# Optimization experiments

Measured on AMD Instinct MI355X. Metric: run time of the kernel, lower is better.

The kernel has to match this reference:

```python
import jax, jax.numpy as jnp
import numpy as np

H, HID = 2, 64
N_USER, N_POST, N_ENT = 50000, 100000, 20000
EDGES = [("publish", 100000, N_USER, N_POST), ("repost", 200000, N_USER, N_POST), ("contain", 200000, N_POST, N_ENT), ("interact", 400000, N_USER, N_USER), ("follow", 400000, N_USER, N_USER), ("similar", 250000, N_POST, N_POST)]


def setup_inputs() -> dict:
    key = jax.random.key(0)
    ks = iter(jax.random.split(key, 64))
    d = {}
    d["x_post"] = jax.random.normal(next(ks), (N_POST, 768), jnp.float32)
    d["x_user"] = jax.random.normal(next(ks), (N_USER, 32), jnp.float32)
    d["x_entity"] = jax.random.normal(next(ks), (N_ENT, 64), jnp.float32)
    for name, E, ns, nd in EDGES:
        d["src_" + name] = jax.random.randint(next(ks), (E,), 0, ns, jnp.int32)
        d["dst_" + name] = jax.random.randint(next(ks), (E,), 0, nd, jnp.int32)
    def lin(k, o, i):
        return jax.random.normal(k, (o, i), jnp.float32) / np.sqrt(i)
    d["post_proj_w"] = lin(next(ks), HID, 768); d["post_proj_b"] = jnp.zeros((HID,), jnp.float32)
    d["user_proj_w"] = lin(next(ks), HID, 32); d["user_proj_b"] = jnp.zeros((HID,), jnp.float32)
    d["ent_proj_w"] = lin(next(ks), HID, 64); d["ent_proj_b"] = jnp.zeros((HID,), jnp.float32)
    # 2 layers x 6 relations of bipartite GATConv params, stacked
    d["W_src"] = jax.random.normal(next(ks), (2, 6, H * HID, HID), jnp.float32) / np.sqrt(HID)
    d["W_dst"] = jax.random.normal(next(ks), (2, 6, H * HID, HID), jnp.float32) / np.sqrt(HID)
    d["a_src"] = jax.random.normal(next(ks), (2, 6, H, HID), jnp.float32) * 0.1
    d["a_dst"] = jax.random.normal(next(ks), (2, 6, H, HID), jnp.float32) * 0.1
    d["gat_b"] = jnp.zeros((2, 6, HID), jnp.float32)
    d["cls_w1"] = lin(next(ks), HID // 2, HID); d["cls_b1"] = jnp.zeros((HID // 2,), jnp.float32)
    d["cls_w2"] = lin(next(ks), 1, HID // 2); d["cls_b2"] = jnp.zeros((1,), jnp.float32)
    return d


def _gat(x_src, x_dst, src, dst, w_s, w_d, a_s, a_d, b):
    """PyG GATConv, bipartite, heads=H, concat=False, no self loops."""
    n_dst = x_dst.shape[0]
    hs = (x_src @ w_s.T).reshape(-1, H, HID)   # [N_src, H, C]
    hd = (x_dst @ w_d.T).reshape(-1, H, HID)   # [N_dst, H, C]
    al_s = jnp.einsum("nhc,hc->nh", hs, a_s)
    al_d = jnp.einsum("nhc,hc->nh", hd, a_d)
    e = jax.nn.leaky_relu(al_s[src] + al_d[dst], negative_slope=0.2)  # [E, H]
    m = jax.ops.segment_max(e, dst, num_segments=n_dst)
    m = jnp.where(jnp.isfinite(m), m, 0.0)  # empty segments -> -inf, unused
    p = jnp.exp(e - m[dst])
    s = jax.ops.segment_sum(p, dst, num_segments=n_dst)
    alpha = p / (s[dst] + 1e-16)
    out = jax.ops.segment_sum(hs[src] * alpha[:, :, None], dst, num_segments=n_dst)
    return out.mean(axis=1) + b  # concat=False -> mean over heads, plus bias


def reference(x_post, x_user, x_entity, src_publish, dst_publish, src_repost, dst_repost, src_contain, dst_contain, src_interact, dst_interact, src_follow, dst_follow, src_similar, dst_similar, post_proj_w, post_proj_b, user_proj_w, user_proj_b, ent_proj_w, ent_proj_b, W_src, W_dst, a_src, a_dst, gat_b, cls_w1, cls_b1, cls_w2, cls_b2):
    h_post = x_post @ post_proj_w.T + post_proj_b
    h_user = x_user @ user_proj_w.T + user_proj_b
    h_ent = x_entity @ ent_proj_w.T + ent_proj_b
    for l in range(2):
        def g(r, xs, xd, s, dd):
            return _gat(xs, xd, s, dd, W_src[l, r], W_dst[l, r], a_src[l, r], a_dst[l, r], gat_b[l, r])
        new_post = (g(0, h_user, h_post, src_publish, dst_publish)
                    + g(1, h_user, h_post, src_repost, dst_repost)
                    + g(5, h_post, h_post, src_similar, dst_similar))
        new_ent = g(2, h_post, h_ent, src_contain, dst_contain)
        new_user = (g(3, h_user, h_user, src_interact, dst_interact)
                    + g(4, h_user, h_user, src_follow, dst_follow))
        h_post, h_user, h_ent = jax.nn.relu(new_post), jax.nn.relu(new_user), jax.nn.relu(new_ent)
    h = jax.nn.relu(h_post @ cls_w1.T + cls_b1)  # dropout is eval-mode identity
    return (h @ cls_w2.T + cls_b2).squeeze(-1)
```

## Files before the change

kernel.cpp:

```cpp
#include <hip/hip_runtime.h>

#define NPOST 100000
#define NUSER 50000
#define NENT  20000
#define NDTOT 420000
#define ETOT  1550000
#define NSCANBLK 206
#define NT_AL 150000

typedef short short8 __attribute__((ext_vector_type(8)));
typedef float f32x4 __attribute__((ext_vector_type(4)));
typedef unsigned short ushort4v __attribute__((ext_vector_type(4)));

static __device__ __forceinline__ unsigned short f2bf(float x){
  union { float f; unsigned u; } v; v.f = x;
  unsigned r = v.u + 0x7FFF + ((v.u >> 16) & 1);
  return (unsigned short)(r >> 16);
}
static __device__ __forceinline__ float bf2f(unsigned short h){
  union { unsigned u; float f; } v; v.u = ((unsigned)h) << 16;
  return v.f;
}

struct EdgeMeta {
  const int* src[6];
  const int* dst[6];
  int E[6];
  int degoff[6];
};

struct PrepArgs {
  const float *Wp, *Wu, *We, *Wsrc, *Wdst, *asrc, *adst, *gatb;
  unsigned short *WpH, *WpL, *WuH, *WuL, *WeH, *WeL, *lbH, *lbL;
  float *weff_s, *weff_d, *bsum;
};

__global__ void k_prep(PrepArgs P){
  int idx = blockIdx.x * blockDim.x + threadIdx.x;
  if (idx < 49152){
    float x = P.Wp[idx];
    unsigned short h = f2bf(x);
    P.WpH[idx] = h; P.WpL[idx] = f2bf(x - bf2f(h));
  } else if (idx < 51200){
    int i = idx - 49152;
    float x = P.Wu[i];
    unsigned short h = f2bf(x);
    P.WuH[i] = h; P.WuL[i] = f2bf(x - bf2f(h));
  } else if (idx < 55296){
    int i = idx - 51200;
    float x = P.We[i];
    unsigned short h = f2bf(x);
    P.WeH[i] = h; P.WeL[i] = f2bf(x - bf2f(h));
  } else if (idx < 153600){
    int i = idx - 55296;
    const int off[6]  = {0, 24576, 40960, 49152, 73728, 90112};
    const int Ks[6]   = {384, 256, 128, 384, 256, 128};
    int seg = 5;
    #pragma unroll
    for (int s = 4; s >= 0; s--) if (i < off[s + 1]) seg = s;
    int l = seg / 3, type = seg % 3;
    int K = Ks[seg];
    int rem = i - off[seg];
    int n = rem / K, k = rem - n * K;
    int slot = k >> 7, head = (k >> 6) & 1, kk = k & 63;
    int rel;
    if (type == 0)      rel = (slot == 0) ? 0 : (slot == 1 ? 1 : 5);
    else if (type == 1) rel = (slot == 0) ? 3 : 4;
    else                rel = 2;
    int m = l * 6 + rel;
    float x = P.Wsrc[(size_t)m * 8192 + (head * 64 + n) * 64 + kk];
    unsigned short h = f2bf(x);
    P.lbH[i] = h; P.lbL[i] = f2bf(x - bf2f(h));
  } else if (idx < 156672){
    int i = idx - 153600;
    const float* W; const float* a; float* o; int j;
    if (i < 1536){ W = P.Wsrc; a = P.asrc; o = P.weff_s; j = i; }
    else         { W = P.Wdst; a = P.adst; o = P.weff_d; j = i - 1536; }
    int m = j >> 7;
    int rem = j & 127;
    int hh = rem >> 6, k = rem & 63;
    const float* Wm = W + (size_t)m * 8192;
    const float* am = a + (size_t)m * 128;
    float acc = 0.f;
    #pragma unroll 8
    for (int c = 0; c < 64; c++)
      acc += Wm[(hh * 64 + c) * 64 + k] * am[hh * 64 + c];
    o[j] = acc;
  } else if (idx < 157056){
    int i = idx - 156672;
    int c = i & 63;
    int lt = i >> 6;
    int l = lt / 3, t = lt % 3;
    float v;
    if (t == 0)      v = P.gatb[(l*6+0)*64+c] + P.gatb[(l*6+1)*64+c] + P.gatb[(l*6+5)*64+c];
    else if (t == 1) v = P.gatb[(l*6+3)*64+c] + P.gatb[(l*6+4)*64+c];
    else             v = P.gatb[(l*6+2)*64+c];
    P.bsum[lt * 64 + c] = v;
  }
}


__global__ void k_hist(EdgeMeta em, int* __restrict__ deg){
  int r = blockIdx.y;
  int e = blockIdx.x * blockDim.x + threadIdx.x;
  if (e >= em.E[r]) return;
  atomicAdd(&deg[em.degoff[r] + em.dst[r][e]], 1);
}

__global__ __launch_bounds__(256) void k_scanA(const int* __restrict__ deg,
                                               int* __restrict__ rowstart,
                                               int* __restrict__ blocksum){
  __shared__ int sums[256];
  int t = threadIdx.x;
  int base = blockIdx.x * 2048 + t * 8;
  int v[8]; int s = 0;
  #pragma unroll
  for (int i = 0; i < 8; i++){
    int j = base + i;
    v[i] = (j < NDTOT) ? deg[j] : 0;
    s += v[i];
  }
  sums[t] = s;
  __syncthreads();
  for (int off = 1; off < 256; off <<= 1){
    int x = (t >= off) ? sums[t - off] : 0;
    __syncthreads();
    sums[t] += x;
    __syncthreads();
  }
  int excl = (t > 0) ? sums[t - 1] : 0;
  if (t == 255) blocksum[blockIdx.x] = sums[255];
  int run = excl;
  #pragma unroll
  for (int i = 0; i < 8; i++){
    int j = base + i;
    if (j < NDTOT) rowstart[j] = run;
    run += v[i];
  }
}

__global__ __launch_bounds__(256) void k_scanB(int* __restrict__ blocksum){
  __shared__ int s[256];
  int t = threadIdx.x;
  s[t] = (t < NSCANBLK) ? blocksum[t] : 0;
  __syncthreads();
  for (int off = 1; off < 256; off <<= 1){
    int x = (t >= off) ? s[t - off] : 0;
    __syncthreads();
    s[t] += x;
    __syncthreads();
  }
  int excl = (t > 0) ? s[t - 1] : 0;
  if (t < NSCANBLK) blocksum[t] = excl;
}

__global__ void k_scanC(int* __restrict__ rowstart, const int* __restrict__ blocksum,
                        int* __restrict__ cursor){
  int j = blockIdx.x * blockDim.x + threadIdx.x;
  if (j < NDTOT){
    int v = rowstart[j] + blocksum[j >> 11];
    rowstart[j] = v;
    cursor[j] = v;
  }
  if (j == 0) rowstart[NDTOT] = ETOT;
}

__global__ void k_scatter(EdgeMeta em, int* __restrict__ cursor,
                          int* __restrict__ csr_src, int* __restrict__ csr_row){
  int r = blockIdx.y;
  int e = blockIdx.x * blockDim.x + threadIdx.x;
  if (e >= em.E[r]) return;
  int d = em.dst[r][e];
  int w = em.degoff[r] + d;
  int pos = atomicAdd(&cursor[w], 1);
  csr_src[pos] = em.src[r][e];
  csr_row[pos] = w;
}


struct AlArgs {
  const float *h0, *h1;
  const float *ws, *wd;
  float *als, *ald;
  int layer;
};

static __device__ __forceinline__ float2 dot2w(const float4* hr, const float* __restrict__ w){
  const float4* w0 = (const float4*)w;
  const float4* w1 = (const float4*)(w + 64);
  float a0 = 0.f, a1 = 0.f;
  #pragma unroll
  for (int q = 0; q < 16; q++){
    float4 v = hr[q];
    float4 x0 = w0[q], x1 = w1[q];
    a0 += v.x*x0.x + v.y*x0.y + v.z*x0.z + v.w*x0.w;
    a1 += v.x*x1.x + v.y*x1.y + v.z*x1.z + v.w*x1.w;
  }
  return make_float2(a0, a1);
}

__global__ __launch_bounds__(256) void k_al_all(AlArgs A){
  int i = blockIdx.x * blockDim.x + threadIdx.x;
  if (i >= NT_AL) return;
  float4 hr[16];
  if (i < NPOST){
    int n = i;
    const float4* hp = (const float4*)(A.h0 + (size_t)n * 64);
    #pragma unroll
    for (int q = 0; q < 16; q++) hr[q] = hp[q];
    *(float2*)(A.als + (size_t)(300000 + n) * 2) = dot2w(hr, A.ws + 5 * 128);
    *(float2*)(A.ald + (size_t)(0      + n) * 2) = dot2w(hr, A.wd + 0 * 128);
    *(float2*)(A.ald + (size_t)(100000 + n) * 2) = dot2w(hr, A.wd + 1 * 128);
    *(float2*)(A.ald + (size_t)(320000 + n) * 2) = dot2w(hr, A.wd + 5 * 128);
  } else {
    int n = i - NPOST;
    const float4* hp = (const float4*)(A.h1 + (size_t)n * 64);
    #pragma unroll
    for (int q = 0; q < 16; q++) hr[q] = hp[q];
    *(float2*)(A.als + (size_t)(0      + n) * 2) = dot2w(hr, A.ws + 0 * 128);
    *(float2*)(A.als + (size_t)(50000  + n) * 2) = dot2w(hr, A.ws + 1 * 128);
    if (A.layer == 0){
      *(float2*)(A.als + (size_t)(200000 + n) * 2) = dot2w(hr, A.ws + 3 * 128);
      *(float2*)(A.als + (size_t)(250000 + n) * 2) = dot2w(hr, A.ws + 4 * 128);
      *(float2*)(A.ald + (size_t)(220000 + n) * 2) = dot2w(hr, A.wd + 3 * 128);
      *(float2*)(A.ald + (size_t)(270000 + n) * 2) = dot2w(hr, A.wd + 4 * 128);
    }
  }
}


struct EdgepArgs {
  const int *csr_src, *csr_row;
  const float *als, *ald;
  float2 *pcsr;
  int thr, off, nE;
};

__global__ __launch_bounds__(256) void k_edgep(EdgepArgs A){
  int e0 = blockIdx.x * blockDim.x + threadIdx.x;
  if (e0 >= A.nE) return;
  int e = e0 < A.thr ? e0 : e0 + A.off;
  int w = A.csr_row[e];
  int soffr;
  if      (w < 100000) soffr = 0;
  else if (w < 200000) soffr = 50000;
  else if (w < 220000) soffr = 100000;
  else if (w < 270000) soffr = 200000;
  else if (w < 320000) soffr = 250000;
  else                 soffr = 300000;
  int sidx = A.csr_src[e];
  float2 as = *(const float2*)(A.als + (size_t)(soffr + sidx) * 2);
  float2 ad = *(const float2*)(A.ald + (size_t)w * 2);
  float e0v = as.x + ad.x, e1v = as.y + ad.y;
  e0v = e0v > 0.f ? e0v : 0.2f * e0v;
  e1v = e1v > 0.f ? e1v : 0.2f * e1v;
  A.pcsr[e] = make_float2(__expf(e0v), __expf(e1v));
}


struct AggArgs {
  const int *rowstart, *csr_src;
  const float *h0, *h1;
  const float2 *pcsr;
  unsigned short *aH0, *aH1, *aL0, *aL1;
  int nrows, thr, off;
};

__global__ __launch_bounds__(256) void k_agg4(AggArgs A){
  int wv = (blockIdx.x * blockDim.x + threadIdx.x) >> 6;
  int lane = threadIdx.x & 63;
  int g = lane >> 4;
  int l16 = lane & 15;
  int r = wv * 4 + g;
  if (r >= A.nrows) return;
  int w = r < A.thr ? r : r + A.off;
  int dgor, slotr, stt, dtt;
  if      (w < 100000){ dgor = 0;      stt = 1; dtt = 0; slotr = 0; }
  else if (w < 200000){ dgor = 100000; stt = 1; dtt = 0; slotr = 1; }
  else if (w < 270000){ dgor = 220000; stt = 1; dtt = 1; slotr = 0; }
  else if (w < 320000){ dgor = 270000; stt = 1; dtt = 1; slotr = 1; }
  else                { dgor = 320000; stt = 0; dtt = 0; slotr = 2; }
  int row = w - dgor;
  const float* h = (stt == 0) ? A.h0 : A.h1;
  int rs = A.rowstart[w], re = A.rowstart[w + 1];
  f32x4 a0 = (f32x4){0.f,0.f,0.f,0.f};
  f32x4 a1 = (f32x4){0.f,0.f,0.f,0.f};
  float s0 = 0.f, s1 = 0.f;
  int e = rs;
  for (; e + 3 < re; e += 4){
    int sa = A.csr_src[e];
    int sb = A.csr_src[e + 1];
    int sc = A.csr_src[e + 2];
    int sd = A.csr_src[e + 3];
    float2 pa = A.pcsr[e];
    float2 pb = A.pcsr[e + 1];
    float2 pc = A.pcsr[e + 2];
    float2 pd = A.pcsr[e + 3];
    f32x4 ha = *(const f32x4*)(h + (size_t)sa * 64 + l16 * 4);
    f32x4 hb = *(const f32x4*)(h + (size_t)sb * 64 + l16 * 4);
    f32x4 hc = *(const f32x4*)(h + (size_t)sc * 64 + l16 * 4);
    f32x4 hd = *(const f32x4*)(h + (size_t)sd * 64 + l16 * 4);
    #pragma unroll
    for (int j = 0; j < 4; j++){
      a0[j] = fmaf(pa.x, ha[j], a0[j]);
      a1[j] = fmaf(pa.y, ha[j], a1[j]);
    }
    s0 += pa.x; s1 += pa.y;
    #pragma unroll
    for (int j = 0; j < 4; j++){
      a0[j] = fmaf(pb.x, hb[j], a0[j]);
      a1[j] = fmaf(pb.y, hb[j], a1[j]);
    }
    s0 += pb.x; s1 += pb.y;
    #pragma unroll
    for (int j = 0; j < 4; j++){
      a0[j] = fmaf(pc.x, hc[j], a0[j]);
      a1[j] = fmaf(pc.y, hc[j], a1[j]);
    }
    s0 += pc.x; s1 += pc.y;
    #pragma unroll
    for (int j = 0; j < 4; j++){
      a0[j] = fmaf(pd.x, hd[j], a0[j]);
      a1[j] = fmaf(pd.y, hd[j], a1[j]);
    }
    s0 += pd.x; s1 += pd.y;
  }
  for (; e + 1 < re; e += 2){
    int sa = A.csr_src[e];
    int sb = A.csr_src[e + 1];
    float2 pa = A.pcsr[e];
    float2 pb = A.pcsr[e + 1];
    f32x4 ha = *(const f32x4*)(h + (size_t)sa * 64 + l16 * 4);
    f32x4 hb = *(const f32x4*)(h + (size_t)sb * 64 + l16 * 4);
    #pragma unroll
    for (int j = 0; j < 4; j++){
      a0[j] = fmaf(pa.x, ha[j], a0[j]);
      a1[j] = fmaf(pa.y, ha[j], a1[j]);
    }
    s0 += pa.x; s1 += pa.y;
    #pragma unroll
    for (int j = 0; j < 4; j++){
      a0[j] = fmaf(pb.x, hb[j], a0[j]);
      a1[j] = fmaf(pb.y, hb[j], a1[j]);
    }
    s0 += pb.x; s1 += pb.y;
  }
  if (e < re){
    int sa = A.csr_src[e];
    float2 pa = A.pcsr[e];
    f32x4 ha = *(const f32x4*)(h + (size_t)sa * 64 + l16 * 4);
    #pragma unroll
    for (int j = 0; j < 4; j++){
      a0[j] = fmaf(pa.x, ha[j], a0[j]);
      a1[j] = fmaf(pa.y, ha[j], a1[j]);
    }
    s0 += pa.x; s1 += pa.y;
  }
  float r0 = s0 > 0.f ? 0.5f / s0 : 0.f;
  float r1 = s1 > 0.f ? 0.5f / s1 : 0.f;
  int K = (dtt == 0) ? 384 : 256;
  unsigned short* aH = (dtt == 0) ? A.aH0 : A.aH1;
  unsigned short* aL = (dtt == 0) ? A.aL0 : A.aL1;
  size_t base = (size_t)row * K + slotr * 128 + l16 * 4;
  ushort4v H0, H1, L0, L1;
  #pragma unroll
  for (int j = 0; j < 4; j++){
    float v0 = a0[j] * r0;
    float v1 = a1[j] * r1;
    unsigned short h0 = f2bf(v0); H0[j] = h0; L0[j] = f2bf(v0 - bf2f(h0));
    unsigned short h1 = f2bf(v1); H1[j] = h1; L1[j] = f2bf(v1 - bf2f(h1));
  }
  *(ushort4v*)(aH + base)      = H0;
  *(ushort4v*)(aH + base + 64) = H1;
  *(ushort4v*)(aL + base)      = L0;
  *(ushort4v*)(aL + base + 64) = L1;
}


static __device__ __forceinline__ int swz(int row, int k){
  return row * 32 + ((((k >> 3) ^ ((row >> 2) & 3))) << 3) + (k & 7);
}

struct GemmJob {
  const float* A32;
  const unsigned short* AH; const unsigned short* AL;
  const unsigned short* BH; const unsigned short* BL;
  const float* bias; float* C;
  int N; int K;
};
struct GemmJobs { GemmJob j0, j1, j2; int nb0, nb1; };

template<int ASRC, int RELU>
__global__ __launch_bounds__(256) void k_mfgemm3(GemmJobs G){
  __shared__ __align__(16) unsigned short sAh[128 * 32];
  __shared__ __align__(16) unsigned short sAl[128 * 32];
  __shared__ __align__(16) unsigned short sBh[64 * 32];
  __shared__ __align__(16) unsigned short sBl[64 * 32];
  int b = blockIdx.x;
  GemmJob jb = G.j0;
  int boff = 0;
  if (b >= G.nb1){ jb = G.j2; boff = G.nb1; }
  else if (b >= G.nb0){ jb = G.j1; boff = G.nb0; }
  const float* A32 = jb.A32;
  const unsigned short* AH = jb.AH;
  const unsigned short* AL = jb.AL;
  const unsigned short* BH = jb.BH;
  const unsigned short* BL = jb.BL;
  int N = jb.N, K = jb.K;

  int t = threadIdx.x;
  int w = t >> 6, lane = t & 63;
  int q = lane >> 4, m15 = lane & 15;
  int r0 = (b - boff) * 128;
  f32x4 acc[2][4];
  #pragma unroll
  for (int i = 0; i < 2; i++)
    #pragma unroll
    for (int j = 0; j < 4; j++)
      acc[i][j] = (f32x4){0.f, 0.f, 0.f, 0.f};

  int arow = t >> 1, akb = (t & 1) * 16;
  int brow = t >> 2, bkb = (t & 3) * 8;

  for (int k0 = 0; k0 < K; k0 += 32){
    int gr = r0 + arow;
    if (ASRC == 0){
      float v[16];
      if (gr < N){
        const float4* ap = (const float4*)(A32 + (size_t)gr * K + k0 + akb);
        #pragma unroll
        for (int i = 0; i < 4; i++){
          float4 f = ap[i];
          v[i*4+0] = f.x; v[i*4+1] = f.y; v[i*4+2] = f.z; v[i*4+3] = f.w;
        }
      } else {
        #pragma unroll
        for (int i = 0; i < 16; i++) v[i] = 0.f;
      }
      short8 h0, h1, l0, l1;
      #pragma unroll
      for (int i = 0; i < 8; i++){
        unsigned short hh = f2bf(v[i]);
        h0[i] = (short)hh; l0[i] = (short)f2bf(v[i] - bf2f(hh));
        unsigned short hj = f2bf(v[8+i]);
        h1[i] = (short)hj; l1[i] = (short)f2bf(v[8+i] - bf2f(hj));
      }
      *(short8*)(sAh + swz(arow, akb))     = h0;
      *(short8*)(sAh + swz(arow, akb + 8)) = h1;
      *(short8*)(sAl + swz(arow, akb))     = l0;
      *(short8*)(sAl + swz(arow, akb + 8)) = l1;
    } else {
      short8 h0 = {0,0,0,0,0,0,0,0}, h1 = {0,0,0,0,0,0,0,0};
      short8 l0 = {0,0,0,0,0,0,0,0}, l1 = {0,0,0,0,0,0,0,0};
      if (gr < N){
        const short8* hp = (const short8*)(AH + (size_t)gr * K + k0 + akb);
        const short8* lp = (const short8*)(AL + (size_t)gr * K + k0 + akb);
        h0 = hp[0]; h1 = hp[1];
        l0 = lp[0]; l1 = lp[1];
      }
      *(short8*)(sAh + swz(arow, akb))     = h0;
      *(short8*)(sAh + swz(arow, akb + 8)) = h1;
      *(short8*)(sAl + swz(arow, akb))     = l0;
      *(short8*)(sAl + swz(arow, akb + 8)) = l1;
    }
    {
      short8 bh = *(const short8*)(BH + (size_t)brow * K + k0 + bkb);
      short8 bl = *(const short8*)(BL + (size_t)brow * K + k0 + bkb);
      *(short8*)(sBh + swz(brow, bkb)) = bh;
      *(short8*)(sBl + swz(brow, bkb)) = bl;
    }
    __syncthreads();
    short8 ah[2], al_[2];
    #pragma unroll
    for (int i = 0; i < 2; i++){
      int mrow = w * 32 + i * 16 + m15;
      ah[i]  = *(const short8*)(sAh + swz(mrow, q * 8));
      al_[i] = *(const short8*)(sAl + swz(mrow, q * 8));
    }
    #pragma unroll
    for (int j = 0; j < 4; j++){
      int bn = j * 16 + m15;
      short8 bh = *(const short8*)(sBh + swz(bn, q * 8));
      short8 bl = *(const short8*)(sBl + swz(bn, q * 8));
      #pragma unroll
      for (int i = 0; i < 2; i++){
        acc[i][j] = __builtin_amdgcn_mfma_f32_16x16x32_bf16(ah[i],  bh, acc[i][j], 0, 0, 0);
        acc[i][j] = __builtin_amdgcn_mfma_f32_16x16x32_bf16(ah[i],  bl, acc[i][j], 0, 0, 0);
        acc[i][j] = __builtin_amdgcn_mfma_f32_16x16x32_bf16(al_[i], bh, acc[i][j], 0, 0, 0);
      }
    }
    __syncthreads();
  }
  const float* bias = jb.bias;
  float* C = jb.C;
  #pragma unroll
  for (int j = 0; j < 4; j++){
    int col = j * 16 + m15;
    float bv = bias[col];
    #pragma unroll
    for (int i = 0; i < 2; i++){
      #pragma unroll
      for (int r = 0; r < 4; r++){
        int row = r0 + w * 32 + i * 16 + q * 4 + r;
        if (row < N){
          float vv = acc[i][j][r] + bv;
          if (RELU) vv = vv > 0.f ? vv : 0.f;
          C[(size_t)row * 64 + col] = vv;
        }
      }
    }
  }
}


__global__ __launch_bounds__(256) void k_classifier(const float* __restrict__ hpost,
                                                    const float* __restrict__ w1,
                                                    const float* __restrict__ b1,
                                                    const float* __restrict__ w2,
                                                    const float* __restrict__ b2,
                                                    float* __restrict__ out, int N){
  __shared__ float w1s[32 * 64];
  __shared__ float b1s[32];
  __shared__ float w2s[32];
  for (int i = threadIdx.x; i < 2048; i += 256) w1s[i] = w1[i];
  if (threadIdx.x < 32){
    b1s[threadIdx.x] = b1[threadIdx.x];
    w2s[threadIdx.x] = w2[threadIdx.x];
  }
  __syncthreads();
  float bias2 = b2[0];
  for (int n = blockIdx.x * blockDim.x + threadIdx.x; n < N; n += gridDim.x * blockDim.x){
    float4 hr[16];
    const float4* hp = (const float4*)(hpost + (size_t)n * 64);
    #pragma unroll
    for (int q = 0; q < 16; q++) hr[q] = hp[q];
    float o = bias2;
    #pragma unroll 4
    for (int j = 0; j < 32; j++){
      float dacc = b1s[j];
      const float4* wr = (const float4*)(w1s + j * 64);
      #pragma unroll
      for (int q = 0; q < 16; q++){
        float4 w = wr[q]; float4 v = hr[q];
        dacc += w.x*v.x + w.y*v.y + w.z*v.z + w.w*v.w;
      }
      dacc = dacc > 0.f ? dacc : 0.f;
      o += w2s[j] * dacc;
    }
    out[n] = o;
  }
}


static inline size_t align256(size_t x){ return (x + 255) & ~(size_t)255; }

extern "C" void kernel_launch(void* const* d_in, const int* in_sizes, int n_in,
                              void* d_out, int out_size, void* d_ws, size_t ws_size,
                              hipStream_t stream){
  (void)in_sizes; (void)n_in; (void)out_size; (void)ws_size;
  const float* x_post = (const float*)d_in[0];
  const float* x_user = (const float*)d_in[1];
  EdgeMeta em;
  for (int r = 0; r < 6; r++){
    em.src[r] = (const int*)d_in[3 + 2*r];
    em.dst[r] = (const int*)d_in[4 + 2*r];
  }
  const int Earr[6] = {100000, 200000, 200000, 400000, 400000, 250000};
  const int dgo[6]  = {0, 100000, 200000, 220000, 270000, 320000};
  for (int r = 0; r < 6; r++){ em.E[r] = Earr[r]; em.degoff[r] = dgo[r]; }

  const float* Wp   = (const float*)d_in[15]; const float* bp = (const float*)d_in[16];
  const float* Wu   = (const float*)d_in[17]; const float* bu = (const float*)d_in[18];
  const float* We   = (const float*)d_in[19];
  const float* Wsrc = (const float*)d_in[21];
  const float* Wdst = (const float*)d_in[22];
  const float* asrc = (const float*)d_in[23];
  const float* adst = (const float*)d_in[24];
  const float* gatb = (const float*)d_in[25];
  const float* cw1  = (const float*)d_in[26]; const float* cb1 = (const float*)d_in[27];
  const float* cw2  = (const float*)d_in[28]; const float* cb2 = (const float*)d_in[29];
  float* out = (float*)d_out;

  const int NN[3] = {NPOST, NUSER, NENT};

  char* p = (char*)d_ws;
  auto alloc = [&](size_t bytes){ char* r = p; p += align256(bytes); return r; };
  float* hA[3]; float* hB[3];
  for (int i = 0; i < 3; i++) hA[i] = (float*)alloc((size_t)NN[i] * 64 * 4);
  for (int i = 0; i < 3; i++) hB[i] = (float*)alloc((size_t)NN[i] * 64 * 4);
  float* als = (float*)alloc((size_t)400000 * 2 * 4);
  float* ald = (float*)alloc((size_t)NDTOT * 2 * 4);
  unsigned short* aggHT[3]; unsigned short* aggLT[3];
  const int KT[3] = {384, 256, 128};
  for (int i = 0; i < 3; i++) aggHT[i] = (unsigned short*)alloc((size_t)NN[i] * KT[i] * 2);
  for (int i = 0; i < 3; i++) aggLT[i] = (unsigned short*)alloc((size_t)NN[i] * KT[i] * 2);
  float* weff_s = (float*)alloc(1536 * 4);
  float* weff_d = (float*)alloc(1536 * 4);
  unsigned short* WpH = (unsigned short*)alloc(768 * 64 * 2);
  unsigned short* WpL = (unsigned short*)alloc(768 * 64 * 2);
  unsigned short* WuH = (unsigned short*)alloc(32 * 64 * 2);
  unsigned short* WuL = (unsigned short*)alloc(32 * 64 * 2);
  unsigned short* WeH = (unsigned short*)alloc(64 * 64 * 2);
  unsigned short* WeL = (unsigned short*)alloc(64 * 64 * 2);
  unsigned short* lbH = (unsigned short*)alloc(98304 * 2);
  unsigned short* lbL = (unsigned short*)alloc(98304 * 2);
  float* bsum   = (float*)alloc(6 * 64 * 4);
  int* deg      = (int*)alloc((size_t)NDTOT * 4);
  int* rowstart = (int*)alloc((size_t)(NDTOT + 1) * 4);
  int* cursor   = (int*)alloc((size_t)NDTOT * 4);
  int* csr_src  = (int*)alloc((size_t)ETOT * 4);
  int* csr_row  = (int*)alloc((size_t)ETOT * 4);
  float2* pcsr  = (float2*)alloc((size_t)ETOT * 8);
  int* blocksum = (int*)alloc((size_t)NSCANBLK * 4);

  hipMemsetAsync(deg, 0, (size_t)NDTOT * 4, stream);
  k_hist<<<dim3(1563, 6), 256, 0, stream>>>(em, deg);
  k_scanA<<<NSCANBLK, 256, 0, stream>>>(deg, rowstart, blocksum);
  k_scanB<<<1, 256, 0, stream>>>(blocksum);
  k_scanC<<<(NDTOT + 255) / 256, 256, 0, stream>>>(rowstart, blocksum, cursor);
  k_scatter<<<dim3(1563, 6), 256, 0, stream>>>(em, cursor, csr_src, csr_row);

  PrepArgs P = {Wp, Wu, We, Wsrc, Wdst, asrc, adst, gatb,
                WpH, WpL, WuH, WuL, WeH, WeL, lbH, lbL,
                weff_s, weff_d, bsum};
  k_prep<<<614, 256, 0, stream>>>(P);

  GemmJobs GP;
  GP.j0 = {x_post, nullptr, nullptr, WpH, WpL, bp, hA[0], NPOST, 768};
  GP.j1 = {x_user, nullptr, nullptr, WuH, WuL, bu, hA[1], NUSER, 32};
  GP.j2 = GP.j1;
  GP.nb0 = 782; GP.nb1 = 1173;
  k_mfgemm3<0, 0><<<1173, 256, 0, stream>>>(GP);

  const int segoff[6] = {0, 24576, 40960, 49152, 73728, 90112};

  float* cur[3] = {hA[0], hA[1], hA[2]};
  float* nxt[3] = {hB[0], hB[1], hB[2]};

  for (int l = 0; l < 2; l++){
    AlArgs AA = {cur[0], cur[1], weff_s + l * 768, weff_d + l * 768, als, ald, l};
    k_al_all<<<(NT_AL + 255) / 256, 256, 0, stream>>>(AA);

    int nE  = (l == 0) ? 1350000 : 550000;
    int eoff = (l == 0) ? 200000 : 1000000;
    EdgepArgs EP = {csr_src, csr_row, als, ald, pcsr, 300000, eoff, nE};
    k_edgep<<<(nE + 255) / 256, 256, 0, stream>>>(EP);

    int nrows = (l == 0) ? 400000 : 300000;
    int roff  = (l == 0) ? 20000 : 120000;
    AggArgs AG = {rowstart, csr_src, cur[0], cur[1], pcsr,
                  aggHT[0], aggHT[1], aggLT[0], aggLT[1], nrows, 200000, roff};
    int aggblocks = (((nrows + 3) / 4) * 64 + 255) / 256;
    k_agg4<<<aggblocks, 256, 0, stream>>>(AG);

    GemmJobs GA;
    GA.j0 = {nullptr, aggHT[0], aggLT[0], lbH + segoff[l*3+0], lbL + segoff[l*3+0],
             bsum + (l*3+0) * 64, nxt[0], NPOST, 384};
    int grid;
    if (l == 0){
      GA.j1 = {nullptr, aggHT[1], aggLT[1], lbH + segoff[l*3+1], lbL + segoff[l*3+1],
               bsum + (l*3+1) * 64, nxt[1], NUSER, 256};
      GA.j2 = GA.j1;
      GA.nb0 = 782; GA.nb1 = 1173; grid = 1173;
    } else {
      GA.j1 = GA.j0; GA.j2 = GA.j0;
      GA.nb0 = 782; GA.nb1 = 782; grid = 782;
    }
    k_mfgemm3<1, 1><<<grid, 256, 0, stream>>>(GA);
    for (int i = 0; i < 2; i++){ float* tmp = cur[i]; cur[i] = nxt[i]; nxt[i] = tmp; }
  }

  k_classifier<<<(NPOST + 255) / 256, 256, 0, stream>>>(cur[0], cw1, cb1, cw2, cb2, out, NPOST);
}
```

Measured before the change: 639.4 us.

## Drop unused contain relation edges and degree-sort aggregation rows

Stops building CSR entries for the post-to-entity 'contain' relation, whose output never reaches the classifier, and removes the entity feature buffers. It also adds a degree counting-sort (histogram, scan, permutation) so the aggregation kernel handles rows grouped by in-degree. Grouping rows of similar degree is meant to reduce wavefront imbalance in the 16-lane-per-row gather. The cost is three extra small kernels and an indirect row lookup that breaks coalesced row order.

Result: slower. 666.9 us (+4.3%).

```diff
diff --git a/kernel.cpp b/kernel.cpp
--- a/kernel.cpp
+++ b/kernel.cpp
@@ -4,9 +4,11 @@
 #define NUSER 50000
 #define NENT  20000
 #define NDTOT 420000
-#define ETOT  1550000
+#define EACT  1350000
 #define NSCANBLK 206
 #define NT_AL 150000
+#define NROW0 400000
+#define NROW1 300000
 
 typedef short short8 __attribute__((ext_vector_type(8)));
 typedef float f32x4 __attribute__((ext_vector_type(4)));
@@ -101,7 +103,8 @@
 
 
 __global__ void k_hist(EdgeMeta em, int* __restrict__ deg){
-  int r = blockIdx.y;
+  const int map[5] = {0, 1, 3, 4, 5};
+  int r = map[blockIdx.y];
   int e = blockIdx.x * blockDim.x + threadIdx.x;
   if (e >= em.E[r]) return;
   atomicAdd(&deg[em.degoff[r] + em.dst[r][e]], 1);
@@ -162,12 +165,13 @@
     rowstart[j] = v;
     cursor[j] = v;
   }
-  if (j == 0) rowstart[NDTOT] = ETOT;
+  if (j == 0) rowstart[NDTOT] = EACT;
 }
 
 __global__ void k_scatter(EdgeMeta em, int* __restrict__ cursor,
                           int* __restrict__ csr_src, int* __restrict__ csr_row){
-  int r = blockIdx.y;
+  const int map[5] = {0, 1, 3, 4, 5};
+  int r = map[blockIdx.y];
   int e = blockIdx.x * blockDim.x + threadIdx.x;
   if (e >= em.E[r]) return;
   int d = em.dst[r][e];
@@ -175,6 +179,76 @@
   int pos = atomicAdd(&cursor[w], 1);
   csr_src[pos] = em.src[r][e];
   csr_row[pos] = w;
+}
+
+
+__global__ __launch_bounds__(256) void k_dhist(const int* __restrict__ rowstart,
+                                               int* __restrict__ bc0, int* __restrict__ bc1){
+  __shared__ int h0[64], h1[64];
+  int t = threadIdx.x;
+  if (t < 64){ h0[t] = 0; h1[t] = 0; }
+  __syncthreads();
+  int i = blockIdx.x * 256 + t;
+  if (i < NROW0){
+    int w = i < 200000 ? i : i + 20000;
+    int d = rowstart[w + 1] - rowstart[w]; d = d > 63 ? 63 : d;
+    atomicAdd(&h0[d], 1);
+  }
+  if (i < NROW1){
+    int w = i < 200000 ? i : i + 120000;
+    int d = rowstart[w + 1] - rowstart[w]; d = d > 63 ? 63 : d;
+    atomicAdd(&h1[d], 1);
+  }
+  __syncthreads();
+  if (t < 64){
+    if (h0[t]) atomicAdd(&bc0[t], h0[t]);
+    if (h1[t]) atomicAdd(&bc1[t], h1[t]);
+  }
+}
+
+__global__ void k_dscan(int* __restrict__ bc0, int* __restrict__ bc1){
+  __shared__ int s0[64], s1[64];
+  int t = threadIdx.x;
+  if (t < 64){ s0[t] = bc0[t]; s1[t] = bc1[t]; }
+  __syncthreads();
+  if (t == 0){
+    int r0 = 0, r1 = 0;
+    for (int i = 0; i < 64; i++){
+      int a = s0[i]; s0[i] = r0; r0 += a;
+      int b = s1[i]; s1[i] = r1; r1 += b;
+    }
+  }
+  __syncthreads();
+  if (t < 64){ bc0[t] = s0[t]; bc1[t] = s1[t]; }
+}
+
+__global__ __launch_bounds__(256) void k_dperm(const int* __restrict__ rowstart,
+                                               int* __restrict__ cur0, int* __restrict__ cur1,
+                                               int* __restrict__ perm0, int* __restrict__ perm1){
+  __shared__ int h0[64], h1[64], b0[64], b1[64];
+  int t = threadIdx.x;
+  if (t < 64){ h0[t] = 0; h1[t] = 0; }
+  __syncthreads();
+  int i = blockIdx.x * 256 + t;
+  int w0 = -1, d0 = 0, lo0 = 0, w1 = -1, d1 = 0, lo1 = 0;
+  if (i < NROW0){
+    w0 = i < 200000 ? i : i + 20000;
+    d0 = rowstart[w0 + 1] - rowstart[w0]; d0 = d0 > 63 ? 63 : d0;
+    lo0 = atomicAdd(&h0[d0], 1);
+  }
+  if (i < NROW1){
+    w1 = i < 200000 ? i : i + 120000;
+    d1 = rowstart[w1 + 1] - rowstart[w1]; d1 = d1 > 63 ? 63 : d1;
+    lo1 = atomicAdd(&h1[d1], 1);
+  }
+  __syncthreads();
+  if (t < 64){
+    b0[t] = h0[t] ? atomicAdd(&cur0[t], h0[t]) : 0;
+    b1[t] = h1[t] ? atomicAdd(&cur1[t], h1[t]) : 0;
+  }
+  __syncthreads();
+  if (w0 >= 0) perm0[b0[d0] + lo0] = w0;
+  if (w1 >= 0) perm1[b1[d1] + lo1] = w1;
 }
 
 
@@ -244,7 +318,6 @@
   int soffr;
   if      (w < 100000) soffr = 0;
   else if (w < 200000) soffr = 50000;
-  else if (w < 220000) soffr = 100000;
   else if (w < 270000) soffr = 200000;
   else if (w < 320000) soffr = 250000;
   else                 soffr = 300000;
@@ -259,11 +332,11 @@
 
 
 struct AggArgs {
-  const int *rowstart, *csr_src;
+  const int *rowstart, *csr_src, *perm;
   const float *h0, *h1;
   const float2 *pcsr;
   unsigned short *aH0, *aH1, *aL0, *aL1;
-  int nrows, thr, off;
+  int nrows;
 };
 
 __global__ __launch_bounds__(256) void k_agg4(AggArgs A){
@@ -273,7 +346,7 @@
   int l16 = lane & 15;
   int r = wv * 4 + g;
   if (r >= A.nrows) return;
-  int w = r < A.thr ? r : r + A.off;
+  int w = A.perm[r];
   int dgor, slotr, stt, dtt;
   if      (w < 100000){ dgor = 0;      stt = 1; dtt = 0; slotr = 0; }
   else if (w < 200000){ dgor = 100000; stt = 1; dtt = 0; slotr = 1; }
@@ -585,15 +658,15 @@
 
   char* p = (char*)d_ws;
   auto alloc = [&](size_t bytes){ char* r = p; p += align256(bytes); return r; };
-  float* hA[3]; float* hB[3];
-  for (int i = 0; i < 3; i++) hA[i] = (float*)alloc((size_t)NN[i] * 64 * 4);
-  for (int i = 0; i < 3; i++) hB[i] = (float*)alloc((size_t)NN[i] * 64 * 4);
+  float* hA[2]; float* hB[2];
+  for (int i = 0; i < 2; i++) hA[i] = (float*)alloc((size_t)NN[i] * 64 * 4);
+  for (int i = 0; i < 2; i++) hB[i] = (float*)alloc((size_t)NN[i] * 64 * 4);
   float* als = (float*)alloc((size_t)400000 * 2 * 4);
   float* ald = (float*)alloc((size_t)NDTOT * 2 * 4);
-  unsigned short* aggHT[3]; unsigned short* aggLT[3];
-  const int KT[3] = {384, 256, 128};
-  for (int i = 0; i < 3; i++) aggHT[i] = (unsigned short*)alloc((size_t)NN[i] * KT[i] * 2);
-  for (int i = 0; i < 3; i++) aggLT[i] = (unsigned short*)alloc((size_t)NN[i] * KT[i] * 2);
+  unsigned short* aggHT[2]; unsigned short* aggLT[2];
+  const int KT[2] = {384, 256};
+  for (int i = 0; i < 2; i++) aggHT[i] = (unsigned short*)alloc((size_t)NN[i] * KT[i] * 2);
+  for (int i = 0; i < 2; i++) aggLT[i] = (unsigned short*)alloc((size_t)NN[i] * KT[i] * 2);
   float* weff_s = (float*)alloc(1536 * 4);
   float* weff_d = (float*)alloc(1536 * 4);
   unsigned short* WpH = (unsigned short*)alloc(768 * 64 * 2);
@@ -608,17 +681,25 @@
   int* deg      = (int*)alloc((size_t)NDTOT * 4);
   int* rowstart = (int*)alloc((size_t)(NDTOT + 1) * 4);
   int* cursor   = (int*)alloc((size_t)NDTOT * 4);
-  int* csr_src  = (int*)alloc((size_t)ETOT * 4);
-  int* csr_row  = (int*)alloc((size_t)ETOT * 4);
-  float2* pcsr  = (float2*)alloc((size_t)ETOT * 8);
+  int* csr_src  = (int*)alloc((size_t)EACT * 4);
+  int* csr_row  = (int*)alloc((size_t)EACT * 4);
+  float2* pcsr  = (float2*)alloc((size_t)EACT * 8);
   int* blocksum = (int*)alloc((size_t)NSCANBLK * 4);
+  int* bc       = (int*)alloc(128 * 4);
+  int* perm0    = (int*)alloc((size_t)NROW0 * 4);
+  int* perm1    = (int*)alloc((size_t)NROW1 * 4);
 
   hipMemsetAsync(deg, 0, (size_t)NDTOT * 4, stream);
-  k_hist<<<dim3(1563, 6), 256, 0, stream>>>(em, deg);
+  hipMemsetAsync(bc, 0, 128 * 4, stream);
+  k_hist<<<dim3(1563, 5), 256, 0, stream>>>(em, deg);
   k_scanA<<<NSCANBLK, 256, 0, stream>>>(deg, rowstart, blocksum);
   k_scanB<<<1, 256, 0, stream>>>(blocksum);
   k_scanC<<<(NDTOT + 255) / 256, 256, 0, stream>>>(rowstart, blocksum, cursor);
-  k_scatter<<<dim3(1563, 6), 256, 0, stream>>>(em, cursor, csr_src, csr_row);
+  k_scatter<<<dim3(1563, 5), 256, 0, stream>>>(em, cursor, csr_src, csr_row);
+
+  k_dhist<<<(NROW0 + 255) / 256, 256, 0, stream>>>(rowstart, bc, bc + 64);
+  k_dscan<<<1, 64, 0, stream>>>(bc, bc + 64);
+  k_dperm<<<(NROW0 + 255) / 256, 256, 0, stream>>>(rowstart, bc, bc + 64, perm0, perm1);
 
   PrepArgs P = {Wp, Wu, We, Wsrc, Wdst, asrc, adst, gatb,
                 WpH, WpL, WuH, WuL, WeH, WeL, lbH, lbL,
@@ -634,22 +715,23 @@
 
   const int segoff[6] = {0, 24576, 40960, 49152, 73728, 90112};
 
-  float* cur[3] = {hA[0], hA[1], hA[2]};
-  float* nxt[3] = {hB[0], hB[1], hB[2]};
+  float* cur[2] = {hA[0], hA[1]};
+  float* nxt[2] = {hB[0], hB[1]};
 
   for (int l = 0; l < 2; l++){
     AlArgs AA = {cur[0], cur[1], weff_s + l * 768, weff_d + l * 768, als, ald, l};
     k_al_all<<<(NT_AL + 255) / 256, 256, 0, stream>>>(AA);
 
-    int nE  = (l == 0) ? 1350000 : 550000;
-    int eoff = (l == 0) ? 200000 : 1000000;
-    EdgepArgs EP = {csr_src, csr_row, als, ald, pcsr, 300000, eoff, nE};
+    int nE  = (l == 0) ? EACT : 550000;
+    int thr = (l == 0) ? EACT : 300000;
+    int off = (l == 0) ? 0 : 800000;
+    EdgepArgs EP = {csr_src, csr_row, als, ald, pcsr, thr, off, nE};
     k_edgep<<<(nE + 255) / 256, 256, 0, stream>>>(EP);
 
-    int nrows = (l == 0) ? 400000 : 300000;
-    int roff  = (l == 0) ? 20000 : 120000;
-    AggArgs AG = {rowstart, csr_src, cur[0], cur[1], pcsr,
-                  aggHT[0], aggHT[1], aggLT[0], aggLT[1], nrows, 200000, roff};
+    int nrows = (l == 0) ? NROW0 : NROW1;
+    const int* perm = (l == 0) ? perm0 : perm1;
+    AggArgs AG = {rowstart, csr_src, perm, cur[0], cur[1], pcsr,
+                  aggHT[0], aggHT[1], aggLT[0], aggLT[1], nrows};
     int aggblocks = (((nrows + 3) / 4) * 64 + 255) / 256;
     k_agg4<<<aggblocks, 256, 0, stream>>>(AG);
 
```

## Fuse edge aggregation with MFMA projection and drop unused contain relation

Applied to the files above, without the earlier changes.

Aggregation and the post-aggregation GEMM are merged into one kernel. Each block aggregates 64 destination rows per slot into swizzled LDS as split bf16 hi/lo tiles, then runs MFMA against the projection weights, adding bias and ReLU at the end. This removes the global round trip of the aggregated hi/lo buffers and a separate kernel launch. The contain relation and entity features are dropped entirely because the output depends only on post nodes, which removes their histogram, scatter, edge and aggregation work. In exchange, B weights are read from global inside the inner loop and blocks sync between gather and GEMM phases, which may lower gather occupancy.

Result: faster. 583.0 us (-8.8%).

```diff
diff --git a/kernel.cpp b/kernel.cpp
--- a/kernel.cpp
+++ b/kernel.cpp
@@ -4,7 +4,7 @@
 #define NUSER 50000
 #define NENT  20000
 #define NDTOT 420000
-#define ETOT  1550000
+#define EACT  1350000
 #define NSCANBLK 206
 #define NT_AL 150000
 
@@ -101,7 +101,8 @@
 
 
 __global__ void k_hist(EdgeMeta em, int* __restrict__ deg){
-  int r = blockIdx.y;
+  const int map[5] = {0, 1, 3, 4, 5};
+  int r = map[blockIdx.y];
   int e = blockIdx.x * blockDim.x + threadIdx.x;
   if (e >= em.E[r]) return;
   atomicAdd(&deg[em.degoff[r] + em.dst[r][e]], 1);
@@ -162,12 +163,13 @@
     rowstart[j] = v;
     cursor[j] = v;
   }
-  if (j == 0) rowstart[NDTOT] = ETOT;
+  if (j == 0) rowstart[NDTOT] = EACT;
 }
 
 __global__ void k_scatter(EdgeMeta em, int* __restrict__ cursor,
                           int* __restrict__ csr_src, int* __restrict__ csr_row){
-  int r = blockIdx.y;
+  const int map[5] = {0, 1, 3, 4, 5};
+  int r = map[blockIdx.y];
   int e = blockIdx.x * blockDim.x + threadIdx.x;
   if (e >= em.E[r]) return;
   int d = em.dst[r][e];
@@ -244,7 +246,6 @@
   int soffr;
   if      (w < 100000) soffr = 0;
   else if (w < 200000) soffr = 50000;
-  else if (w < 220000) soffr = 100000;
   else if (w < 270000) soffr = 200000;
   else if (w < 320000) soffr = 250000;
   else                 soffr = 300000;
@@ -258,122 +259,174 @@
 }
 
 
-struct AggArgs {
-  const int *rowstart, *csr_src;
-  const float *h0, *h1;
-  const float2 *pcsr;
-  unsigned short *aH0, *aH1, *aL0, *aL1;
-  int nrows, thr, off;
-};
-
-__global__ __launch_bounds__(256) void k_agg4(AggArgs A){
-  int wv = (blockIdx.x * blockDim.x + threadIdx.x) >> 6;
-  int lane = threadIdx.x & 63;
-  int g = lane >> 4;
-  int l16 = lane & 15;
-  int r = wv * 4 + g;
-  if (r >= A.nrows) return;
-  int w = r < A.thr ? r : r + A.off;
-  int dgor, slotr, stt, dtt;
-  if      (w < 100000){ dgor = 0;      stt = 1; dtt = 0; slotr = 0; }
-  else if (w < 200000){ dgor = 100000; stt = 1; dtt = 0; slotr = 1; }
-  else if (w < 270000){ dgor = 220000; stt = 1; dtt = 1; slotr = 0; }
-  else if (w < 320000){ dgor = 270000; stt = 1; dtt = 1; slotr = 1; }
-  else                { dgor = 320000; stt = 0; dtt = 0; slotr = 2; }
-  int row = w - dgor;
-  const float* h = (stt == 0) ? A.h0 : A.h1;
-  int rs = A.rowstart[w], re = A.rowstart[w + 1];
-  f32x4 a0 = (f32x4){0.f,0.f,0.f,0.f};
-  f32x4 a1 = (f32x4){0.f,0.f,0.f,0.f};
-  float s0 = 0.f, s1 = 0.f;
+static __device__ __forceinline__ int aswz(int row, int k){
+  return row * 128 + ((((k >> 3) ^ (row & 7))) << 3) + (k & 7);
+}
+
+static __device__ __forceinline__ void agg_row(const int* __restrict__ csr_src,
+                                               const float2* __restrict__ pcsr,
+                                               const float* __restrict__ h, int l16,
+                                               int rs, int re,
+                                               f32x4& a0, f32x4& a1, float& s0, float& s1){
   int e = rs;
   for (; e + 3 < re; e += 4){
-    int sa = A.csr_src[e];
-    int sb = A.csr_src[e + 1];
-    int sc = A.csr_src[e + 2];
-    int sd = A.csr_src[e + 3];
-    float2 pa = A.pcsr[e];
-    float2 pb = A.pcsr[e + 1];
-    float2 pc = A.pcsr[e + 2];
-    float2 pd = A.pcsr[e + 3];
+    int sa = csr_src[e];
+    int sb = csr_src[e + 1];
+    int sc = csr_src[e + 2];
+    int sd = csr_src[e + 3];
+    float2 pa = pcsr[e];
+    float2 pb = pcsr[e + 1];
+    float2 pc = pcsr[e + 2];
+    float2 pd = pcsr[e + 3];
     f32x4 ha = *(const f32x4*)(h + (size_t)sa * 64 + l16 * 4);
     f32x4 hb = *(const f32x4*)(h + (size_t)sb * 64 + l16 * 4);
     f32x4 hc = *(const f32x4*)(h + (size_t)sc * 64 + l16 * 4);
     f32x4 hd = *(const f32x4*)(h + (size_t)sd * 64 + l16 * 4);
     #pragma unroll
-    for (int j = 0; j < 4; j++){
-      a0[j] = fmaf(pa.x, ha[j], a0[j]);
-      a1[j] = fmaf(pa.y, ha[j], a1[j]);
-    }
+    for (int j = 0; j < 4; j++){ a0[j] = fmaf(pa.x, ha[j], a0[j]); a1[j] = fmaf(pa.y, ha[j], a1[j]); }
     s0 += pa.x; s1 += pa.y;
     #pragma unroll
-    for (int j = 0; j < 4; j++){
-      a0[j] = fmaf(pb.x, hb[j], a0[j]);
-      a1[j] = fmaf(pb.y, hb[j], a1[j]);
-    }
+    for (int j = 0; j < 4; j++){ a0[j] = fmaf(pb.x, hb[j], a0[j]); a1[j] = fmaf(pb.y, hb[j], a1[j]); }
     s0 += pb.x; s1 += pb.y;
     #pragma unroll
-    for (int j = 0; j < 4; j++){
-      a0[j] = fmaf(pc.x, hc[j], a0[j]);
-      a1[j] = fmaf(pc.y, hc[j], a1[j]);
-    }
+    for (int j = 0; j < 4; j++){ a0[j] = fmaf(pc.x, hc[j], a0[j]); a1[j] = fmaf(pc.y, hc[j], a1[j]); }
     s0 += pc.x; s1 += pc.y;
     #pragma unroll
-    for (int j = 0; j < 4; j++){
-      a0[j] = fmaf(pd.x, hd[j], a0[j]);
-      a1[j] = fmaf(pd.y, hd[j], a1[j]);
-    }
+    for (int j = 0; j < 4; j++){ a0[j] = fmaf(pd.x, hd[j], a0[j]); a1[j] = fmaf(pd.y, hd[j], a1[j]); }
     s0 += pd.x; s1 += pd.y;
   }
   for (; e + 1 < re; e += 2){
-    int sa = A.csr_src[e];
-    int sb = A.csr_src[e + 1];
-    float2 pa = A.pcsr[e];
-    float2 pb = A.pcsr[e + 1];
+    int sa = csr_src[e];
+    int sb = csr_src[e + 1];
+    float2 pa = pcsr[e];
+    float2 pb = pcsr[e + 1];
     f32x4 ha = *(const f32x4*)(h + (size_t)sa * 64 + l16 * 4);
     f32x4 hb = *(const f32x4*)(h + (size_t)sb * 64 + l16 * 4);
     #pragma unroll
-    for (int j = 0; j < 4; j++){
-      a0[j] = fmaf(pa.x, ha[j], a0[j]);
-      a1[j] = fmaf(pa.y, ha[j], a1[j]);
-    }
+    for (int j = 0; j < 4; j++){ a0[j] = fmaf(pa.x, ha[j], a0[j]); a1[j] = fmaf(pa.y, ha[j], a1[j]); }
     s0 += pa.x; s1 += pa.y;
     #pragma unroll
-    for (int j = 0; j < 4; j++){
-      a0[j] = fmaf(pb.x, hb[j], a0[j]);
-      a1[j] = fmaf(pb.y, hb[j], a1[j]);
-    }
+    for (int j = 0; j < 4; j++){ a0[j] = fmaf(pb.x, hb[j], a0[j]); a1[j] = fmaf(pb.y, hb[j], a1[j]); }
     s0 += pb.x; s1 += pb.y;
   }
   if (e < re){
-    int sa = A.csr_src[e];
-    float2 pa = A.pcsr[e];
+    int sa = csr_src[e];
+    float2 pa = pcsr[e];
     f32x4 ha = *(const f32x4*)(h + (size_t)sa * 64 + l16 * 4);
     #pragma unroll
-    for (int j = 0; j < 4; j++){
-      a0[j] = fmaf(pa.x, ha[j], a0[j]);
-      a1[j] = fmaf(pa.y, ha[j], a1[j]);
-    }
+    for (int j = 0; j < 4; j++){ a0[j] = fmaf(pa.x, ha[j], a0[j]); a1[j] = fmaf(pa.y, ha[j], a1[j]); }
     s0 += pa.x; s1 += pa.y;
   }
-  float r0 = s0 > 0.f ? 0.5f / s0 : 0.f;
-  float r1 = s1 > 0.f ? 0.5f / s1 : 0.f;
-  int K = (dtt == 0) ? 384 : 256;
-  unsigned short* aH = (dtt == 0) ? A.aH0 : A.aH1;
-  unsigned short* aL = (dtt == 0) ? A.aL0 : A.aL1;
-  size_t base = (size_t)row * K + slotr * 128 + l16 * 4;
-  ushort4v H0, H1, L0, L1;
+}
+
+struct FJob {
+  const unsigned short *BH, *BL;
+  const float *bias;
+  float *C;
+  int N, nslots, K;
+  int wb0, wb1, wb2;
+  int ss0, ss1, ss2;
+};
+struct FArgs {
+  const int *rowstart, *csr_src;
+  const float2 *pcsr;
+  const float *h0, *h1;
+  FJob j0, j1;
+  int nb0;
+};
+
+__global__ __launch_bounds__(256) void k_fused(FArgs A){
+  __shared__ __align__(16) unsigned short sAh[64 * 128];
+  __shared__ __align__(16) unsigned short sAl[64 * 128];
+  int b = blockIdx.x;
+  FJob J = (b < A.nb0) ? A.j0 : A.j1;
+  int boff = (b < A.nb0) ? 0 : A.nb0;
+  int r0 = (b - boff) * 64;
+  int t = threadIdx.x;
+  int w = t >> 6, lane = t & 63;
+  int q = lane >> 4, m15 = lane & 15;
+  int g2 = t >> 4, l16 = t & 15;
+  int wr = w & 1, wc = w >> 1;
+  f32x4 acc[2][2];
   #pragma unroll
-  for (int j = 0; j < 4; j++){
-    float v0 = a0[j] * r0;
-    float v1 = a1[j] * r1;
-    unsigned short h0 = f2bf(v0); H0[j] = h0; L0[j] = f2bf(v0 - bf2f(h0));
-    unsigned short h1 = f2bf(v1); H1[j] = h1; L1[j] = f2bf(v1 - bf2f(h1));
-  }
-  *(ushort4v*)(aH + base)      = H0;
-  *(ushort4v*)(aH + base + 64) = H1;
-  *(ushort4v*)(aL + base)      = L0;
-  *(ushort4v*)(aL + base + 64) = L1;
+  for (int i = 0; i < 2; i++)
+    #pragma unroll
+    for (int j = 0; j < 2; j++)
+      acc[i][j] = (f32x4){0.f, 0.f, 0.f, 0.f};
+
+  for (int s = 0; s < J.nslots; s++){
+    int wbase = (s == 0) ? J.wb0 : ((s == 1) ? J.wb1 : J.wb2);
+    int ssel  = (s == 0) ? J.ss0 : ((s == 1) ? J.ss1 : J.ss2);
+    const float* h = ssel ? A.h1 : A.h0;
+    for (int rr = g2; rr < 64; rr += 16){
+      int grow = r0 + rr;
+      int rs = 0, re = 0;
+      if (grow < J.N){
+        int wg = wbase + grow;
+        rs = A.rowstart[wg];
+        re = A.rowstart[wg + 1];
+      }
+      f32x4 a0 = (f32x4){0.f,0.f,0.f,0.f};
+      f32x4 a1 = (f32x4){0.f,0.f,0.f,0.f};
+      float s0 = 0.f, s1 = 0.f;
+      agg_row(A.csr_src, A.pcsr, h, l16, rs, re, a0, a1, s0, s1);
+      float r0v = s0 > 0.f ? 0.5f / s0 : 0.f;
+      float r1v = s1 > 0.f ? 0.5f / s1 : 0.f;
+      ushort4v H0, H1, L0, L1;
+      #pragma unroll
+      for (int j = 0; j < 4; j++){
+        float v0 = a0[j] * r0v;
+        float v1 = a1[j] * r1v;
+        unsigned short h0v = f2bf(v0); H0[j] = h0v; L0[j] = f2bf(v0 - bf2f(h0v));
+        unsigned short h1v = f2bf(v1); H1[j] = h1v; L1[j] = f2bf(v1 - bf2f(h1v));
+      }
+      *(ushort4v*)(sAh + aswz(rr, l16 * 4))      = H0;
+      *(ushort4v*)(sAh + aswz(rr, 64 + l16 * 4)) = H1;
+      *(ushort4v*)(sAl + aswz(rr, l16 * 4))      = L0;
+      *(ushort4v*)(sAl + aswz(rr, 64 + l16 * 4)) = L1;
+    }
+    __syncthreads();
+    #pragma unroll
+    for (int kc = 0; kc < 4; kc++){
+      int gk = s * 128 + kc * 32;
+      short8 ah[2], al_[2];
+      #pragma unroll
+      for (int i = 0; i < 2; i++){
+        int mrow = wr * 32 + i * 16 + m15;
+        ah[i]  = *(const short8*)(sAh + aswz(mrow, kc * 32 + q * 8));
+        al_[i] = *(const short8*)(sAl + aswz(mrow, kc * 32 + q * 8));
+      }
+      #pragma unroll
+      for (int j = 0; j < 2; j++){
+        int bn = wc * 32 + j * 16 + m15;
+        short8 bh = *(const short8*)(J.BH + (size_t)bn * J.K + gk + q * 8);
+        short8 bl = *(const short8*)(J.BL + (size_t)bn * J.K + gk + q * 8);
+        #pragma unroll
+        for (int i = 0; i < 2; i++){
+          acc[i][j] = __builtin_amdgcn_mfma_f32_16x16x32_bf16(ah[i],  bh, acc[i][j], 0, 0, 0);
+          acc[i][j] = __builtin_amdgcn_mfma_f32_16x16x32_bf16(ah[i],  bl, acc[i][j], 0, 0, 0);
+          acc[i][j] = __builtin_amdgcn_mfma_f32_16x16x32_bf16(al_[i], bh, acc[i][j], 0, 0, 0);
+        }
+      }
+    }
+    __syncthreads();
+  }
+  #pragma unroll
+  for (int j = 0; j < 2; j++){
+    int col = wc * 32 + j * 16 + m15;
+    float bv = J.bias[col];
+    #pragma unroll
+    for (int i = 0; i < 2; i++){
+      #pragma unroll
+      for (int r = 0; r < 4; r++){
+        int row = r0 + wr * 32 + i * 16 + q * 4 + r;
+        if (row < J.N){
+          float vv = acc[i][j][r] + bv;
+          J.C[(size_t)row * 64 + col] = vv > 0.f ? vv : 0.f;
+        }
+      }
+    }
+  }
 }
 
 
@@ -581,19 +634,15 @@
   const float* cw2  = (const float*)d_in[28]; const float* cb2 = (const float*)d_in[29];
   float* out = (float*)d_out;
 
-  const int NN[3] = {NPOST, NUSER, NENT};
+  const int NN[2] = {NPOST, NUSER};
 
   char* p = (char*)d_ws;
   auto alloc = [&](size_t bytes){ char* r = p; p += align256(bytes); return r; };
-  float* hA[3]; float* hB[3];
-  for (int i = 0; i < 3; i++) hA[i] = (float*)alloc((size_t)NN[i] * 64 * 4);
-  for (int i = 0; i < 3; i++) hB[i] = (float*)alloc((size_t)NN[i] * 64 * 4);
+  float* hA[2]; float* hB[2];
+  for (int i = 0; i < 2; i++) hA[i] = (float*)alloc((size_t)NN[i] * 64 * 4);
+  for (int i = 0; i < 2; i++) hB[i] = (float*)alloc((size_t)NN[i] * 64 * 4);
   float* als = (float*)alloc((size_t)400000 * 2 * 4);
   float* ald = (float*)alloc((size_t)NDTOT * 2 * 4);
-  unsigned short* aggHT[3]; unsigned short* aggLT[3];
-  const int KT[3] = {384, 256, 128};
-  for (int i = 0; i < 3; i++) aggHT[i] = (unsigned short*)alloc((size_t)NN[i] * KT[i] * 2);
-  for (int i = 0; i < 3; i++) aggLT[i] = (unsigned short*)alloc((size_t)NN[i] * KT[i] * 2);
   float* weff_s = (float*)alloc(1536 * 4);
   float* weff_d = (float*)alloc(1536 * 4);
   unsigned short* WpH = (unsigned short*)alloc(768 * 64 * 2);
@@ -608,17 +657,17 @@
   int* deg      = (int*)alloc((size_t)NDTOT * 4);
   int* rowstart = (int*)alloc((size_t)(NDTOT + 1) * 4);
   int* cursor   = (int*)alloc((size_t)NDTOT * 4);
-  int* csr_src  = (int*)alloc((size_t)ETOT * 4);
-  int* csr_row  = (int*)alloc((size_t)ETOT * 4);
-  float2* pcsr  = (float2*)alloc((size_t)ETOT * 8);
+  int* csr_src  = (int*)alloc((size_t)EACT * 4);
+  int* csr_row  = (int*)alloc((size_t)EACT * 4);
+  float2* pcsr  = (float2*)alloc((size_t)EACT * 8);
   int* blocksum = (int*)alloc((size_t)NSCANBLK * 4);
 
   hipMemsetAsync(deg, 0, (size_t)NDTOT * 4, stream);
-  k_hist<<<dim3(1563, 6), 256, 0, stream>>>(em, deg);
+  k_hist<<<dim3(1563, 5), 256, 0, stream>>>(em, deg);
   k_scanA<<<NSCANBLK, 256, 0, stream>>>(deg, rowstart, blocksum);
   k_scanB<<<1, 256, 0, stream>>>(blocksum);
   k_scanC<<<(NDTOT + 255) / 256, 256, 0, stream>>>(rowstart, blocksum, cursor);
-  k_scatter<<<dim3(1563, 6), 256, 0, stream>>>(em, cursor, csr_src, csr_row);
+  k_scatter<<<dim3(1563, 5), 256, 0, stream>>>(em, cursor, csr_src, csr_row);
 
   PrepArgs P = {Wp, Wu, We, Wsrc, Wdst, asrc, adst, gatb,
                 WpH, WpL, WuH, WuL, WeH, WeL, lbH, lbL,
@@ -634,39 +683,35 @@
 
   const int segoff[6] = {0, 24576, 40960, 49152, 73728, 90112};
 
-  float* cur[3] = {hA[0], hA[1], hA[2]};
-  float* nxt[3] = {hB[0], hB[1], hB[2]};
+  float* cur[2] = {hA[0], hA[1]};
+  float* nxt[2] = {hB[0], hB[1]};
 
   for (int l = 0; l < 2; l++){
     AlArgs AA = {cur[0], cur[1], weff_s + l * 768, weff_d + l * 768, als, ald, l};
     k_al_all<<<(NT_AL + 255) / 256, 256, 0, stream>>>(AA);
 
-    int nE  = (l == 0) ? 1350000 : 550000;
-    int eoff = (l == 0) ? 200000 : 1000000;
-    EdgepArgs EP = {csr_src, csr_row, als, ald, pcsr, 300000, eoff, nE};
+    int nE  = (l == 0) ? EACT : 550000;
+    int thr = (l == 0) ? EACT : 300000;
+    int off = (l == 0) ? 0 : 800000;
+    EdgepArgs EP = {csr_src, csr_row, als, ald, pcsr, thr, off, nE};
     k_edgep<<<(nE + 255) / 256, 256, 0, stream>>>(EP);
 
-    int nrows = (l == 0) ? 400000 : 300000;
-    int roff  = (l == 0) ? 20000 : 120000;
-    AggArgs AG = {rowstart, csr_src, cur[0], cur[1], pcsr,
-                  aggHT[0], aggHT[1], aggLT[0], aggLT[1], nrows, 200000, roff};
-    int aggblocks = (((nrows + 3) / 4) * 64 + 255) / 256;
-    k_agg4<<<aggblocks, 256, 0, stream>>>(AG);
-
-    GemmJobs GA;
-    GA.j0 = {nullptr, aggHT[0], aggLT[0], lbH + segoff[l*3+0], lbL + segoff[l*3+0],
-             bsum + (l*3+0) * 64, nxt[0], NPOST, 384};
+    FArgs FA;
+    FA.rowstart = rowstart; FA.csr_src = csr_src; FA.pcsr = pcsr;
+    FA.h0 = cur[0]; FA.h1 = cur[1];
+    FA.j0 = {lbH + segoff[l*3+0], lbL + segoff[l*3+0], bsum + (l*3+0) * 64, nxt[0],
+             NPOST, 3, 384, 0, 100000, 320000, 1, 1, 0};
     int grid;
     if (l == 0){
-      GA.j1 = {nullptr, aggHT[1], aggLT[1], lbH + segoff[l*3+1], lbL + segoff[l*3+1],
-               bsum + (l*3+1) * 64, nxt[1], NUSER, 256};
-      GA.j2 = GA.j1;
-      GA.nb0 = 782; GA.nb1 = 1173; grid = 1173;
+      FA.j1 = {lbH + segoff[l*3+1], lbL + segoff[l*3+1], bsum + (l*3+1) * 64, nxt[1],
+               NUSER, 2, 256, 220000, 270000, 0, 1, 1, 0};
+      FA.nb0 = 1563; grid = 1563 + 782;
     } else {
-      GA.j1 = GA.j0; GA.j2 = GA.j0;
-      GA.nb0 = 782; GA.nb1 = 782; grid = 782;
-    }
-    k_mfgemm3<1, 1><<<grid, 256, 0, stream>>>(GA);
+      FA.j1 = FA.j0;
+      FA.nb0 = 1563; grid = 1563;
+    }
+    k_fused<<<grid, 256, 0, stream>>>(FA);
+
     for (int i = 0; i < 2; i++){ float* tmp = cur[i]; cur[i] = nxt[i]; nxt[i] = tmp; }
   }
 
```
